# Performance work log

Measured on AMD Instinct MI355X. Metric: run time of the kernel, lower is better.

The kernel has to match this reference:

```python
import jax, jax.numpy as jnp
import numpy as np
from jax import lax

KSIZE = 7
SIGMA = 1.0  # torchvision samples sigma~U(0.1,2.0); fixed here for determinism


def _gauss_kernel():
    x = jnp.arange(KSIZE, dtype=jnp.float32) - (KSIZE - 1) / 2
    k = jnp.exp(-0.5 * (x / SIGMA) ** 2)
    return k / k.sum()


def gaussian_blur(img):
    # img: [B, C, H, W]; separable 7x7 Gaussian, reflect padding (torchvision behavior)
    B, C, H, W = img.shape
    k = _gauss_kernel()
    p = KSIZE // 2
    img = jnp.pad(img, ((0, 0), (0, 0), (p, p), (p, p)), mode='reflect')
    kh = jnp.tile(k.reshape(1, 1, KSIZE, 1), (C, 1, 1, 1))  # depthwise vertical
    kw = jnp.tile(k.reshape(1, 1, 1, KSIZE), (C, 1, 1, 1))  # depthwise horizontal
    dn = ('NCHW', 'OIHW', 'NCHW')
    img = lax.conv_general_dilated(img, kh, (1, 1), 'VALID', feature_group_count=C, dimension_numbers=dn)
    img = lax.conv_general_dilated(img, kw, (1, 1), 'VALID', feature_group_count=C, dimension_numbers=dn)
    return img  # [B, C, H, W]


def sample_bilinear_border(img, pos):
    # img: [B, C, H, W]; pos: [B, L, 2] (x, y) in [0, 1].
    # Equivalent to F.grid_sample(img, 2*pos-1, align_corners=False, padding_mode='border')
    # WITHOUT materializing the (bs*L)-repeated image.
    B, C, H, W = img.shape
    gx = 2.0 * pos[..., 0] - 1.0
    gy = 2.0 * pos[..., 1] - 1.0
    # align_corners=False unnormalization, then border clamp
    x = jnp.clip(((gx + 1.0) * W - 1.0) * 0.5, 0.0, W - 1)
    y = jnp.clip(((gy + 1.0) * H - 1.0) * 0.5, 0.0, H - 1)
    x0f = jnp.floor(x); y0f = jnp.floor(y)
    wx = (x - x0f)[..., None]  # [B, L, 1]
    wy = (y - y0f)[..., None]
    x0 = x0f.astype(jnp.int32); y0 = y0f.astype(jnp.int32)
    x1 = jnp.minimum(x0 + 1, W - 1); y1 = jnp.minimum(y0 + 1, H - 1)
    b = jnp.arange(B)[:, None]  # [B, 1] broadcasts with [B, L] indices
    v00 = img[b, :, y0, x0]  # [B, L, C]
    v01 = img[b, :, y0, x1]
    v10 = img[b, :, y1, x0]
    v11 = img[b, :, y1, x1]
    return (v00 * (1 - wx) * (1 - wy) + v01 * wx * (1 - wy)
            + v10 * (1 - wx) * wy + v11 * wx * wy)


def setup_inputs() -> dict:
    key = jax.random.key(0)
    k1, k2 = jax.random.split(key)
    predictions = jax.random.uniform(k1, (32, 64, 8), dtype=jnp.float32)
    ref_imgs = jax.random.uniform(k2, (32, 3, 512, 512), dtype=jnp.float32)
    return {"predictions": predictions, "ref_imgs": ref_imgs}


def reference(predictions, ref_imgs):
    pos = lax.stop_gradient(predictions[:, :, :2])   # grid is .detach()'d in the original
    color = predictions[:, :, 5:]                    # [B, L, 3]
    blurred = gaussian_blur(ref_imgs)
    target = sample_bilinear_border(blurred, pos)    # [B, L, 3]
    return jnp.mean((color - target) ** 2)           # MSELoss ('l2')
```

## Files before the change

### kernel.cpp

```cpp
#include <hip/hip_runtime.h>


#define IMG_H 512
#define IMG_W 512
#define NELEM 6144
#define NBLOCKS 24

__device__ __forceinline__ int refl(int i, int n) {
    if (i < 0) i = -i;
    if (i >= n) i = 2 * n - 2 - i;
    return i;
}

__global__ __launch_bounds__(256) void loss_kernel(
    const float* __restrict__ pred,
    const float* __restrict__ imgs,
    float* __restrict__ out)
{
    const int tid = blockIdx.x * 256 + threadIdx.x;
    const int c  = tid % 3;
    const int pn = tid / 3;
    const int b  = pn >> 6;

    float kk[7];
    float ks = 0.f;
    #pragma unroll
    for (int j = 0; j < 7; ++j) {
        float xx = (float)j - 3.0f;
        kk[j] = expf(-0.5f * xx * xx);
        ks += kk[j];
    }
    #pragma unroll
    for (int j = 0; j < 7; ++j) kk[j] /= ks;

    const float* p = pred + pn * 8;
    const float px = p[0], py = p[1];

    float gx = 2.f * px - 1.f;
    float gy = 2.f * py - 1.f;
    float x = ((gx + 1.f) * (float)IMG_W - 1.f) * 0.5f;
    float y = ((gy + 1.f) * (float)IMG_H - 1.f) * 0.5f;
    x = fminf(fmaxf(x, 0.f), (float)(IMG_W - 1));
    y = fminf(fmaxf(y, 0.f), (float)(IMG_H - 1));
    const float x0f = floorf(x), y0f = floorf(y);
    const float wx = x - x0f, wy = y - y0f;
    const int x0 = (int)x0f, y0 = (int)y0f;
    const int x1 = min(x0 + 1, IMG_W - 1);
    const int y1 = min(y0 + 1, IMG_H - 1);
    const int dx = x1 - x0;
    const int dy = y1 - y0;

    const float* img = imgs + (size_t)(b * 3 + c) * (IMG_H * IMG_W);

    int cx[8];
    #pragma unroll
    for (int j = 0; j < 8; ++j) cx[j] = refl(x0 - 3 + j, IMG_W);

    float h0[8], h1[8];
    #pragma unroll
    for (int r = 0; r < 8; ++r) {
        const int iy = refl(y0 - 3 + r, IMG_H);
        const float* row = img + iy * IMG_W;
        float w[8];
        #pragma unroll
        for (int j = 0; j < 8; ++j) w[j] = row[cx[j]];
        float s0 = 0.f, s1 = 0.f;
        #pragma unroll
        for (int j = 0; j < 7; ++j) {
            s0 += kk[j] * w[j];
            s1 += kk[j] * w[j + dx];
        }
        h0[r] = s0; h1[r] = s1;
    }

    float v00 = 0.f, v01 = 0.f, v10 = 0.f, v11 = 0.f;
    #pragma unroll
    for (int j = 0; j < 7; ++j) {
        v00 += kk[j] * h0[j];
        v01 += kk[j] * h1[j];
        v10 += kk[j] * h0[j + dy];
        v11 += kk[j] * h1[j + dy];
    }

    const float target = v00 * (1.f - wx) * (1.f - wy)
                       + v01 * wx         * (1.f - wy)
                       + v10 * (1.f - wx) * wy
                       + v11 * wx         * wy;

    const float color = p[5 + c];
    const float d = color - target;
    float val = d * d;

    #pragma unroll
    for (int off = 32; off > 0; off >>= 1)
        val += __shfl_down(val, off, 64);

    __shared__ float sm[4];
    const int lane = threadIdx.x & 63;
    const int wave = threadIdx.x >> 6;
    if (lane == 0) sm[wave] = val;
    __syncthreads();
    if (threadIdx.x == 0) {
        const float blocksum = sm[0] + sm[1] + sm[2] + sm[3];
        atomicAdd(out, blocksum * (1.0f / (float)NELEM));
    }
}

extern "C" void kernel_launch(void* const* d_in, const int* in_sizes, int n_in,
                              void* d_out, int out_size, void* d_ws, size_t ws_size,
                              hipStream_t stream) {
    const float* pred = (const float*)d_in[0];
    const float* imgs = (const float*)d_in[1];
    float* out = (float*)d_out;

    loss_kernel<<<NBLOCKS, 256, 0, stream>>>(pred, imgs, out);
}
```

Before: 143.5 us.

## Split each sample's 8 blur rows across 8 lanes with shuffle reduction

Each (point, channel) output is now computed by 8 threads, one per source row of the 8x8 footprint, instead of a single thread looping over all rows. Horizontal partial sums are weighted by the vertical taps per lane and combined with xor-shuffles. The grid grows from 24 to 192 blocks so the latency-bound gather loads are spread over far more waves and CUs. The cost is redundant coordinate and kernel-weight setup in every lane and 8x duplicated squared errors, which the final scale divides out.

After: 129.0 us. -10.1%, faster.

```diff
diff --git a/kernel.cpp b/kernel.cpp
--- a/kernel.cpp
+++ b/kernel.cpp
@@ -4,7 +4,8 @@
 #define IMG_H 512
 #define IMG_W 512
 #define NELEM 6144
-#define NBLOCKS 24
+#define BLOCK 256
+#define NBLOCKS 192
 
 __device__ __forceinline__ int refl(int i, int n) {
     if (i < 0) i = -i;
@@ -17,9 +18,11 @@
     const float* __restrict__ imgs,
     float* __restrict__ out)
 {
-    const int tid = blockIdx.x * 256 + threadIdx.x;
-    const int c  = tid % 3;
-    const int pn = tid / 3;
+    const int t  = blockIdx.x * BLOCK + threadIdx.x;
+    const int r  = t & 7;
+    const int g  = t >> 3;
+    const int c  = g % 3;
+    const int pn = g / 3;
     const int b  = pn >> 6;
 
     float kk[7];
@@ -52,40 +55,38 @@
 
     const float* img = imgs + (size_t)(b * 3 + c) * (IMG_H * IMG_W);
 
-    int cx[8];
+    const int iy = refl(y0 - 3 + r, IMG_H);
+    const float* row = img + iy * IMG_W;
+
+    float w[8];
     #pragma unroll
-    for (int j = 0; j < 8; ++j) cx[j] = refl(x0 - 3 + j, IMG_W);
+    for (int j = 0; j < 8; ++j) w[j] = row[refl(x0 - 3 + j, IMG_W)];
 
-    float h0[8], h1[8];
+    float s0 = 0.f, s1 = 0.f;
     #pragma unroll
-    for (int r = 0; r < 8; ++r) {
-        const int iy = refl(y0 - 3 + r, IMG_H);
-        const float* row = img + iy * IMG_W;
-        float w[8];
-        #pragma unroll
-        for (int j = 0; j < 8; ++j) w[j] = row[cx[j]];
-        float s0 = 0.f, s1 = 0.f;
-        #pragma unroll
-        for (int j = 0; j < 7; ++j) {
-            s0 += kk[j] * w[j];
-            s1 += kk[j] * w[j + dx];
-        }
-        h0[r] = s0; h1[r] = s1;
+    for (int j = 0; j < 7; ++j) {
+        s0 += kk[j] * w[j];
+        s1 += kk[j] * w[j + dx];
     }
 
-    float v00 = 0.f, v01 = 0.f, v10 = 0.f, v11 = 0.f;
+    const float wa = (r < 7) ? kk[r] : 0.f;
+    const int  rb = r - dy;
+    const float wb = (rb >= 0 && rb < 7) ? kk[rb] : 0.f;
+
+    float c00 = wa * s0, c01 = wa * s1;
+    float c10 = wb * s0, c11 = wb * s1;
     #pragma unroll
-    for (int j = 0; j < 7; ++j) {
-        v00 += kk[j] * h0[j];
-        v01 += kk[j] * h1[j];
-        v10 += kk[j] * h0[j + dy];
-        v11 += kk[j] * h1[j + dy];
+    for (int off = 1; off < 8; off <<= 1) {
+        c00 += __shfl_xor(c00, off, 64);
+        c01 += __shfl_xor(c01, off, 64);
+        c10 += __shfl_xor(c10, off, 64);
+        c11 += __shfl_xor(c11, off, 64);
     }
 
-    const float target = v00 * (1.f - wx) * (1.f - wy)
-                       + v01 * wx         * (1.f - wy)
-                       + v10 * (1.f - wx) * wy
-                       + v11 * wx         * wy;
+    const float target = c00 * (1.f - wx) * (1.f - wy)
+                       + c01 * wx         * (1.f - wy)
+                       + c10 * (1.f - wx) * wy
+                       + c11 * wx         * wy;
 
     const float color = p[5 + c];
     const float d = color - target;
@@ -102,7 +103,7 @@
     __syncthreads();
     if (threadIdx.x == 0) {
         const float blocksum = sm[0] + sm[1] + sm[2] + sm[3];
-        atomicAdd(out, blocksum * (1.0f / (float)NELEM));
+        atomicAdd(out, blocksum * (1.0f / (8.0f * (float)NELEM)));
     }
 }
 
@@ -113,5 +114,5 @@
     const float* imgs = (const float*)d_in[1];
     float* out = (float*)d_out;
 
-    loss_kernel<<<NBLOCKS, 256, 0, stream>>>(pred, imgs, out);
+    loss_kernel<<<NBLOCKS, BLOCK, 0, stream>>>(pred, imgs, out);
 }
```
